# Optimization experiments

Measured on AMD Instinct MI355X. Metric: run time of the kernel, lower is better.

Reference implementation:

```python
import jax, jax.numpy as jnp
import numpy as np

EMB_DIM = 768
HEAD = 12
HEAD_DIM = EMB_DIM // HEAD


def setup_inputs() -> dict:
    key = jax.random.key(0)
    ks = jax.random.split(key, 6)
    B, N, D = 8, 1024, EMB_DIM
    s = 1.0 / np.sqrt(D)
    return {
        "z": jax.random.normal(ks[0], (B, N, D), dtype=jnp.float32),
        "w_q": jax.random.normal(ks[1], (D, D), dtype=jnp.float32) * s,
        "w_k": jax.random.normal(ks[2], (D, D), dtype=jnp.float32) * s,
        "w_v": jax.random.normal(ks[3], (D, D), dtype=jnp.float32) * s,
        "w_o": jax.random.normal(ks[4], (D, D), dtype=jnp.float32) * s,
        "b_o": jax.random.normal(ks[5], (D,), dtype=jnp.float32) * 0.01,
    }


def reference(z, w_q, w_k, w_v, w_o, b_o):
    B, N, D = z.shape
    sqrt_dh = jnp.asarray(HEAD_DIM, z.dtype) ** 0.5
    # project and split heads: [B, H, N, Dh]
    def heads(x, w):
        return (x @ w.T).reshape(B, N, HEAD, HEAD_DIM).transpose(0, 2, 1, 3)
    q = heads(z, w_q)
    k = heads(z, w_k)
    v = heads(z, w_v)
    dots = jnp.einsum("bhqd,bhkd->bhqk", q, k) / sqrt_dh
    attn = jax.nn.softmax(dots, axis=-1)  # dropout p=0 -> identity
    out = jnp.einsum("bhqk,bhkd->bhqd", attn, v)
    out = out.transpose(0, 2, 1, 3).reshape(B, N, D)
    return out @ w_o.T + b_o
```

## Files before the change

kernel.cpp:

```cpp
#include <hip/hip_runtime.h>
#include <hip/hip_bf16.h>
#include <stdint.h>

typedef unsigned short u16;
typedef __attribute__((ext_vector_type(8))) short bf16x8;
typedef __attribute__((ext_vector_type(4))) float f32x4;

__device__ __forceinline__ u16 f2bf(float f) {
    union { float f; unsigned int i; } c; c.f = f;
    unsigned int x = c.i;
    return (u16)((x + 0x7FFFu + ((x >> 16) & 1u)) >> 16);
}
__device__ __forceinline__ u16 f2bf_fast(float f) {
    union { float f; unsigned int i; } c; c.f = f;
    return (u16)((c.i + 0x8000u) >> 16);
}

__device__ __forceinline__ void glds16(const u16* g, u16* l) {
    __builtin_amdgcn_global_load_lds(
        (const __attribute__((address_space(1))) void*)g,
        (__attribute__((address_space(3))) void*)l, 16, 0, 0);
}

__device__ __forceinline__ void bar() { asm volatile("s_barrier" ::: "memory"); }
template <int N> __device__ __forceinline__ void waitv() {
    if constexpr (N == 0)      asm volatile("s_waitcnt vmcnt(0)" ::: "memory");
    else if constexpr (N == 2) asm volatile("s_waitcnt vmcnt(2)" ::: "memory");
    else if constexpr (N == 3) asm volatile("s_waitcnt vmcnt(3)" ::: "memory");
    else if constexpr (N == 4) asm volatile("s_waitcnt vmcnt(4)" ::: "memory");
    else if constexpr (N == 8) asm volatile("s_waitcnt vmcnt(8)" ::: "memory");
}

__global__ __launch_bounds__(256) void convert_all(
    const float* __restrict__ z, const float* __restrict__ wq,
    const float* __restrict__ wk, const float* __restrict__ wv,
    const float* __restrict__ wo,
    u16* __restrict__ zb, u16* __restrict__ wqb, u16* __restrict__ wkb,
    u16* __restrict__ wvb, u16* __restrict__ wob)
{
    int g = blockIdx.x * 256 + threadIdx.x;
    const float* s; u16* d;
    if (g < 786432)       { s = z;  d = zb;  }
    else if (g < 860160)  { s = wq; d = wqb; g -= 786432; }
    else if (g < 933888)  { s = wk; d = wkb; g -= 860160; }
    else if (g < 1007616) { s = wv; d = wvb; g -= 933888; }
    else                  { s = wo; d = wob; g -= 1007616; }
    float4 a = *(const float4*)(s + (size_t)g * 8);
    float4 b = *(const float4*)(s + (size_t)g * 8 + 4);
    u16 t[8] = {f2bf(a.x), f2bf(a.y), f2bf(a.z), f2bf(a.w),
                f2bf(b.x), f2bf(b.y), f2bf(b.z), f2bf(b.w)};
    *(uint4*)(d + (size_t)g * 8) = *(const uint4*)t;
}

template <int MI>
__device__ __forceinline__ void gemm_mainloop(
    const u16* __restrict__ A, const u16* __restrict__ B,
    u16* As, u16* Bs, f32x4 (&acc)[MI][4], int m0, int lda, int ldb, int K)
{
    const int t = threadIdx.x;
    const int w = t >> 6, lane = t & 63, quad = lane >> 4, lc = lane & 15;
    const int wm = w >> 1, wn = w & 1;
    const int swz = (lc >> 1) & 3;
    constexpr int NA = MI / 2;
    constexpr int ASZ = 1024 * MI;

    const u16* pa[NA]; int la[NA];
    #pragma unroll
    for (int j = 0; j < NA; j++) {
        const int c = j * 256 + t;
        const int row = c >> 2;
        const int kq = (c & 3) ^ ((row >> 1) & 3);
        pa[j] = &A[(size_t)(m0 + row) * lda + kq * 8];
        la[j] = (j * 256 + w * 64) * 8;
    }
    const u16* pb[2]; int lb[2];
    #pragma unroll
    for (int j = 0; j < 2; j++) {
        const int c = j * 256 + t;
        const int row = c >> 2;
        const int kq = (c & 3) ^ ((row >> 1) & 3);
        pb[j] = &B[(size_t)row * ldb + kq * 8];
        lb[j] = (j * 256 + w * 64) * 8;
    }

    #pragma unroll
    for (int j = 0; j < NA; j++) glds16(pa[j], As + la[j]);
    #pragma unroll
    for (int j = 0; j < 2; j++) glds16(pb[j], Bs + lb[j]);
    __syncthreads();

    int buf = 0;
    for (int k0 = 0; k0 < K; k0 += 32) {
        if (k0 + 32 < K) {
            const int na = (buf ^ 1) * ASZ, nbb = (buf ^ 1) * 4096;
            #pragma unroll
            for (int j = 0; j < NA; j++) glds16(pa[j] + k0 + 32, As + na + la[j]);
            #pragma unroll
            for (int j = 0; j < 2; j++)  glds16(pb[j] + k0 + 32, Bs + nbb + lb[j]);
        }
        bf16x8 af[MI], bfr[4];
        #pragma unroll
        for (int i = 0; i < MI; i++) {
            const int row = 32 * NA * wm + 16 * i + lc;
            af[i] = *(const bf16x8*)&As[buf * ASZ + (row * 4 + (quad ^ swz)) * 8];
        }
        #pragma unroll
        for (int j = 0; j < 4; j++) {
            const int row = 64 * wn + 16 * j + lc;
            bfr[j] = *(const bf16x8*)&Bs[buf * 4096 + (row * 4 + (quad ^ swz)) * 8];
        }
        #pragma unroll
        for (int i = 0; i < MI; i++)
            #pragma unroll
            for (int j = 0; j < 4; j++)
                acc[i][j] = __builtin_amdgcn_mfma_f32_16x16x32_bf16(af[i], bfr[j], acc[i][j], 0, 0, 0);
        __syncthreads();
        buf ^= 1;
    }
}

__global__ __launch_bounds__(256) void qkv_gemm(
    const u16* __restrict__ zb, const u16* __restrict__ wqb,
    const u16* __restrict__ wkb, const u16* __restrict__ wvb,
    u16* __restrict__ qkb, u16* __restrict__ vt)
{
    __shared__ __align__(16) u16 As[8192], Bs[8192];
    const int d = blockIdx.x;
    const int n0 = (d >> 6) * 128, m0 = (d & 63) * 128;
    const u16* Bp;
    if (n0 < 768)       Bp = wqb + (size_t)n0 * 768;
    else if (n0 < 1536) Bp = wkb + (size_t)(n0 - 768) * 768;
    else                Bp = wvb + (size_t)(n0 - 1536) * 768;

    const int t = threadIdx.x;
    const int w = t >> 6, lane = t & 63, quad = lane >> 4, lc = lane & 15;
    const int wm = w >> 1, wn = w & 1;
    const int swz = (lc >> 1) & 3;

    const u16* pa[2]; const u16* pb[2]; int la[2], lb[2];
    #pragma unroll
    for (int j = 0; j < 2; j++) {
        const int c = j * 256 + t;
        const int row = c >> 2;
        const int kq = (c & 3) ^ ((row >> 1) & 3);
        pa[j] = &zb[(size_t)(m0 + row) * 768 + kq * 8];
        pb[j] = &Bp[(size_t)row * 768 + kq * 8];
        la[j] = lb[j] = (j * 256 + w * 64) * 8;
    }

    glds16(pa[0], As + la[0]);  glds16(pa[1], As + la[1]);
    glds16(pb[0], Bs + lb[0]);  glds16(pb[1], Bs + lb[1]);
    glds16(pa[0] + 32, As + 4096 + la[0]);  glds16(pa[1] + 32, As + 4096 + la[1]);
    glds16(pb[0] + 32, Bs + 4096 + lb[0]);  glds16(pb[1] + 32, Bs + 4096 + lb[1]);

    f32x4 acc[4][4] = {};
    int buf = 0;
    for (int bk = 0; bk < 24; bk++) {
        if (bk + 1 < 24) waitv<4>(); else waitv<0>();
        bar();
        bf16x8 af[4], bfr[4];
        #pragma unroll
        for (int i = 0; i < 4; i++) {
            const int row = 64 * wm + 16 * i + lc;
            af[i] = *(const bf16x8*)&As[buf * 4096 + (row * 4 + (quad ^ swz)) * 8];
        }
        #pragma unroll
        for (int j = 0; j < 4; j++) {
            const int row = 64 * wn + 16 * j + lc;
            bfr[j] = *(const bf16x8*)&Bs[buf * 4096 + (row * 4 + (quad ^ swz)) * 8];
        }
        #pragma unroll
        for (int i = 0; i < 4; i++)
            #pragma unroll
            for (int j = 0; j < 4; j++)
                acc[i][j] = __builtin_amdgcn_mfma_f32_16x16x32_bf16(af[i], bfr[j], acc[i][j], 0, 0, 0);
        bar();
        if (bk + 2 < 24) {
            const int k2 = (bk + 2) * 32;
            glds16(pa[0] + k2, As + buf * 4096 + la[0]);
            glds16(pa[1] + k2, As + buf * 4096 + la[1]);
            glds16(pb[0] + k2, Bs + buf * 4096 + lb[0]);
            glds16(pb[1] + k2, Bs + buf * 4096 + lb[1]);
        }
        buf ^= 1;
    }

    if (n0 < 1536) {
        #pragma unroll
        for (int i = 0; i < 4; i++)
            #pragma unroll
            for (int j = 0; j < 4; j++) {
                const int col = n0 + 64 * wn + 16 * j + lc;
                #pragma unroll
                for (int r = 0; r < 4; r++) {
                    const int row = m0 + 64 * wm + 16 * i + quad * 4 + r;
                    qkb[(size_t)row * 1536 + col] = f2bf_fast(acc[i][j][r]);
                }
            }
    } else {
        #pragma unroll
        for (int i = 0; i < 4; i++)
            #pragma unroll
            for (int j = 0; j < 4; j++) {
                const int c = (n0 - 1536) + 64 * wn + 16 * j + lc;
                const int h = c >> 6, dd = c & 63;
                const int tok0 = m0 + 64 * wm + 16 * i + quad * 4;
                const int b = tok0 >> 10, n = tok0 & 1023;
                ushort4 pk = { f2bf_fast(acc[i][j][0]), f2bf_fast(acc[i][j][1]),
                               f2bf_fast(acc[i][j][2]), f2bf_fast(acc[i][j][3]) };
                *(ushort4*)&vt[(((size_t)(b * 12 + h)) * 64 + dd) * 1024 + n] = pk;
            }
    }
}

__global__ __launch_bounds__(256) void oproj_gemm(
    const u16* __restrict__ ob, const u16* __restrict__ wob,
    const float* __restrict__ bo, float* __restrict__ out)
{
    __shared__ __align__(16) u16 As[4096], Bs[8192];
    const int d = blockIdx.x;
    const int n0 = (d >> 7) * 128, m0 = (d & 127) * 64;
    f32x4 acc[2][4] = {};
    gemm_mainloop<2>(ob, wob + (size_t)n0 * 768, As, Bs, acc, m0, 768, 768, 768);

    const int t = threadIdx.x;
    const int w = t >> 6, lane = t & 63, quad = lane >> 4, lc = lane & 15;
    const int wm = w >> 1, wn = w & 1;
    #pragma unroll
    for (int i = 0; i < 2; i++)
        #pragma unroll
        for (int j = 0; j < 4; j++) {
            const int col = n0 + 64 * wn + 16 * j + lc;
            const float bv = bo[col];
            #pragma unroll
            for (int r = 0; r < 4; r++) {
                const int row = m0 + 32 * wm + 16 * i + quad * 4 + r;
                out[(size_t)row * 768 + col] = acc[i][j][r] + bv;
            }
        }
}

__global__ __launch_bounds__(256, 3) void attn_kernel(
    const u16* __restrict__ qkb, const u16* __restrict__ vt,
    u16* __restrict__ obuf)
{
    const int b = blockIdx.x / 12, h = blockIdx.x % 12;
    const int q0 = blockIdx.y * 128;
    const int t = threadIdx.x;
    const int w = t >> 6, lane = t & 63, quad = lane >> 4, lc = lane & 15;

    const u16* Qp  = qkb + (size_t)b * 1024 * 1536 + h * 64;
    const u16* Kp  = Qp + 768;
    const u16* Vtp = vt + ((size_t)(b * 12 + h)) * 64 * 1024;

    __shared__ __align__(16) u16 U[128 * 136];
    __shared__ __align__(16) u16 Vts[64 * 128];

    const u16* kp[4]; u16* kl[4];
    #pragma unroll
    for (int j = 0; j < 4; j++) {
        const int c = j * 256 + t;
        const int row = c >> 3;
        const int kq = (c & 7) ^ ((row >> 1) & 7);
        kp[j] = Kp + (size_t)row * 1536 + kq * 8;
        kl[j] = &U[(j * 256 + w * 64) * 8];
    }
    const u16* vp[4]; u16* vl[4];
    #pragma unroll
    for (int s2 = 0; s2 < 4; s2++) {
        const int s = 4 * w + s2;
        const int c = s * 64 + lane;
        const int dd = c >> 4, kq = (c & 15) ^ (dd & 15);
        vp[s2] = Vtp + (size_t)dd * 1024 + kq * 8;
        vl[s2] = &Vts[s * 512];
    }

    bf16x8 qf[2][2];
    #pragma unroll
    for (int rg = 0; rg < 2; rg++)
        #pragma unroll
        for (int kk = 0; kk < 2; kk++)
            qf[rg][kk] = *(const bf16x8*)&Qp[(size_t)(q0 + 32 * w + 16 * rg + lc) * 1536
                                             + kk * 32 + quad * 8];

    f32x4 oacc[2][4] = {};
    float lsum[2][4] = {};

    const float cs = 0.18033688011112042f;
    const int swk = (lc >> 1) & 7;

    waitv<0>();
    for (int kt = 0; kt < 8; kt++) {
        const int kb = kt * 128;
        bar();
        #pragma unroll
        for (int j = 0; j < 4; j++)
            glds16(kp[j] + (size_t)kb * 1536, kl[j]);
        #pragma unroll
        for (int s2 = 0; s2 < 4; s2++)
            glds16(vp[s2] + kb, vl[s2]);
        waitv<4>();
        bar();

        f32x4 sacc[2][8] = {};
        #pragma unroll
        for (int j = 0; j < 8; j++) {
            const int nrow = 16 * j + lc;
            bf16x8 kf0 = *(const bf16x8*)&U[(nrow * 8 + (quad ^ swk)) * 8];
            bf16x8 kf1 = *(const bf16x8*)&U[(nrow * 8 + ((4 + quad) ^ swk)) * 8];
            #pragma unroll
            for (int rg = 0; rg < 2; rg++) {
                sacc[rg][j] = __builtin_amdgcn_mfma_f32_16x16x32_bf16(qf[rg][0], kf0, sacc[rg][j], 0, 0, 0);
                sacc[rg][j] = __builtin_amdgcn_mfma_f32_16x16x32_bf16(qf[rg][1], kf1, sacc[rg][j], 0, 0, 0);
            }
        }
        waitv<0>();
        bar();

        #pragma unroll
        for (int rg = 0; rg < 2; rg++)
            #pragma unroll
            for (int j = 0; j < 8; j++)
                #pragma unroll
                for (int r = 0; r < 4; r++) {
                    float p = __builtin_amdgcn_exp2f(sacc[rg][j][r] * cs);
                    lsum[rg][r] += p;
                    U[(32 * w + 16 * rg + quad * 4 + r) * 136 + 16 * j + lc] = f2bf_fast(p);
                }

        #pragma unroll
        for (int ks = 0; ks < 4; ks++) {
            bf16x8 pa[2];
            #pragma unroll
            for (int rg = 0; rg < 2; rg++)
                pa[rg] = *(const bf16x8*)&U[(32 * w + 16 * rg + lc) * 136 + ks * 32 + quad * 8];
            #pragma unroll
            for (int jd = 0; jd < 4; jd++) {
                bf16x8 vb = *(const bf16x8*)&Vts[(((16 * jd + lc) << 4) + ((ks * 4 + quad) ^ lc)) * 8];
                #pragma unroll
                for (int rg = 0; rg < 2; rg++)
                    oacc[rg][jd] = __builtin_amdgcn_mfma_f32_16x16x32_bf16(pa[rg], vb, oacc[rg][jd], 0, 0, 0);
            }
        }
    }

    #pragma unroll
    for (int off = 1; off < 16; off <<= 1)
        #pragma unroll
        for (int rg = 0; rg < 2; rg++)
            #pragma unroll
            for (int r = 0; r < 4; r++)
                lsum[rg][r] += __shfl_xor(lsum[rg][r], off, 64);

    float invl[2][4];
    #pragma unroll
    for (int rg = 0; rg < 2; rg++)
        #pragma unroll
        for (int r = 0; r < 4; r++) invl[rg][r] = __builtin_amdgcn_rcpf(lsum[rg][r]);
    #pragma unroll
    for (int rg = 0; rg < 2; rg++)
        #pragma unroll
        for (int jd = 0; jd < 4; jd++)
            #pragma unroll
            for (int r = 0; r < 4; r++) {
                const int row = q0 + 32 * w + 16 * rg + quad * 4 + r;
                const int col = h * 64 + 16 * jd + lc;
                obuf[((size_t)b * 1024 + row) * 768 + col] = f2bf_fast(oacc[rg][jd][r] * invl[rg][r]);
            }
}

extern "C" void kernel_launch(void* const* d_in, const int* in_sizes, int n_in,
                              void* d_out, int out_size, void* d_ws, size_t ws_size,
                              hipStream_t stream) {
    const float* z  = (const float*)d_in[0];
    const float* wq = (const float*)d_in[1];
    const float* wk = (const float*)d_in[2];
    const float* wv = (const float*)d_in[3];
    const float* wo = (const float*)d_in[4];
    const float* bo = (const float*)d_in[5];

    u16* ws16 = (u16*)d_ws;
    u16* zb   = ws16;
    u16* wqb  = zb  + 6291456;
    u16* wkb  = wqb + 589824;
    u16* wvb  = wkb + 589824;
    u16* wob  = wvb + 589824;
    u16* vt   = wob + 589824;
    u16* qkb  = (u16*)d_out;
    u16* obuf = zb;
    float* out = (float*)d_out;

    convert_all<<<4224, 256, 0, stream>>>(z, wq, wk, wv, wo, zb, wqb, wkb, wvb, wob);
    qkv_gemm<<<1152, 256, 0, stream>>>(zb, wqb, wkb, wvb, qkb, vt);
    attn_kernel<<<dim3(96, 8), 256, 0, stream>>>(qkb, vt, obuf);
    oproj_gemm<<<768, 256, 0, stream>>>(obuf, wob, bo, out);
}
```

Before: 193.4 us.

## Shrink attention key tile to 64, double-buffer K, separate P buffer

The attention loop now processes 64-key tiles instead of 128 and double-buffers K in shared memory, prefetching the next K tile while the current one is used. P gets its own XOR-swizzled buffer instead of aliasing the K staging area, and the V tile layout is adjusted to match the smaller tile. Shared memory per block drops, and launch bounds are raised to 4 blocks per CU for more occupancy. This adds twice as many loop iterations and barriers and tighter register pressure.

```diff
diff --git a/kernel.cpp b/kernel.cpp
--- a/kernel.cpp
+++ b/kernel.cpp
@@ -240,7 +240,7 @@
         }
 }
 
-__global__ __launch_bounds__(256, 3) void attn_kernel(
+__global__ __launch_bounds__(256, 4) void attn_kernel(
     const u16* __restrict__ qkb, const u16* __restrict__ vt,
     u16* __restrict__ obuf)
 {
@@ -253,24 +253,25 @@
     const u16* Kp  = Qp + 768;
     const u16* Vtp = vt + ((size_t)(b * 12 + h)) * 64 * 1024;
 
-    __shared__ __align__(16) u16 U[128 * 136];
-    __shared__ __align__(16) u16 Vts[64 * 128];
-
-    const u16* kp[4]; u16* kl[4];
-    #pragma unroll
-    for (int j = 0; j < 4; j++) {
+    __shared__ __align__(16) u16 Ks[2][4096];
+    __shared__ __align__(16) u16 Vts[4096];
+    __shared__ __align__(16) u16 Ps[8192];
+
+    const u16* kp[2]; int kl[2];
+    #pragma unroll
+    for (int j = 0; j < 2; j++) {
         const int c = j * 256 + t;
         const int row = c >> 3;
         const int kq = (c & 7) ^ ((row >> 1) & 7);
         kp[j] = Kp + (size_t)row * 1536 + kq * 8;
-        kl[j] = &U[(j * 256 + w * 64) * 8];
-    }
-    const u16* vp[4]; u16* vl[4];
-    #pragma unroll
-    for (int s2 = 0; s2 < 4; s2++) {
-        const int s = 4 * w + s2;
+        kl[j] = (j * 256 + w * 64) * 8;
+    }
+    const u16* vp[2]; u16* vl[2];
+    #pragma unroll
+    for (int s2 = 0; s2 < 2; s2++) {
+        const int s = 2 * w + s2;
         const int c = s * 64 + lane;
-        const int dd = c >> 4, kq = (c & 15) ^ (dd & 15);
+        const int dd = c >> 3, kq = (c & 7) ^ (dd & 7);
         vp[s2] = Vtp + (size_t)dd * 1024 + kq * 8;
         vl[s2] = &Vts[s * 512];
     }
@@ -288,55 +289,72 @@
 
     const float cs = 0.18033688011112042f;
     const int swk = (lc >> 1) & 7;
+    const int pR0 = 32 * w;
 
     waitv<0>();
-    for (int kt = 0; kt < 8; kt++) {
-        const int kb = kt * 128;
+    glds16(kp[0], &Ks[0][0] + kl[0]);
+    glds16(kp[1], &Ks[0][0] + kl[1]);
+
+    for (int kt = 0; kt < 16; kt++) {
+        const int kb = kt * 64;
         bar();
-        #pragma unroll
-        for (int j = 0; j < 4; j++)
-            glds16(kp[j] + (size_t)kb * 1536, kl[j]);
-        #pragma unroll
-        for (int s2 = 0; s2 < 4; s2++)
-            glds16(vp[s2] + kb, vl[s2]);
-        waitv<4>();
+        glds16(vp[0] + kb, vl[0]);
+        glds16(vp[1] + kb, vl[1]);
+        if (kt + 1 < 16) {
+            const size_t kb1 = (size_t)(kt + 1) * 64 * 1536;
+            u16* kd = &Ks[(kt + 1) & 1][0];
+            glds16(kp[0] + kb1, kd + kl[0]);
+            glds16(kp[1] + kb1, kd + kl[1]);
+            waitv<4>();
+        } else {
+            waitv<2>();
+        }
         bar();
 
-        f32x4 sacc[2][8] = {};
-        #pragma unroll
-        for (int j = 0; j < 8; j++) {
+        const u16* Kc = &Ks[kt & 1][0];
+        f32x4 sacc[2][4] = {};
+        #pragma unroll
+        for (int j = 0; j < 4; j++) {
             const int nrow = 16 * j + lc;
-            bf16x8 kf0 = *(const bf16x8*)&U[(nrow * 8 + (quad ^ swk)) * 8];
-            bf16x8 kf1 = *(const bf16x8*)&U[(nrow * 8 + ((4 + quad) ^ swk)) * 8];
+            bf16x8 kf0 = *(const bf16x8*)&Kc[(nrow * 8 + (quad ^ swk)) * 8];
+            bf16x8 kf1 = *(const bf16x8*)&Kc[(nrow * 8 + ((4 + quad) ^ swk)) * 8];
             #pragma unroll
             for (int rg = 0; rg < 2; rg++) {
                 sacc[rg][j] = __builtin_amdgcn_mfma_f32_16x16x32_bf16(qf[rg][0], kf0, sacc[rg][j], 0, 0, 0);
                 sacc[rg][j] = __builtin_amdgcn_mfma_f32_16x16x32_bf16(qf[rg][1], kf1, sacc[rg][j], 0, 0, 0);
             }
         }
-        waitv<0>();
+        if (kt + 1 < 16) waitv<2>();
+        else             waitv<0>();
         bar();
 
         #pragma unroll
-        for (int rg = 0; rg < 2; rg++)
-            #pragma unroll
-            for (int j = 0; j < 8; j++)
+        for (int rg = 0; rg < 2; rg++) {
+            const int Rb = pR0 + 16 * rg + quad * 4;
+            #pragma unroll
+            for (int j = 0; j < 4; j++)
                 #pragma unroll
                 for (int r = 0; r < 4; r++) {
                     float p = __builtin_amdgcn_exp2f(sacc[rg][j][r] * cs);
                     lsum[rg][r] += p;
-                    U[(32 * w + 16 * rg + quad * 4 + r) * 136 + 16 * j + lc] = f2bf_fast(p);
+                    const int R = Rb + r;
+                    const int slot = (2 * j + (lc >> 3)) ^ ((R >> 1) & 7);
+                    Ps[R * 64 + slot * 8 + (lc & 7)] = f2bf_fast(p);
                 }
-
-        #pragma unroll
-        for (int ks = 0; ks < 4; ks++) {
+        }
+
+        #pragma unroll
+        for (int ks = 0; ks < 2; ks++) {
             bf16x8 pa[2];
             #pragma unroll
-            for (int rg = 0; rg < 2; rg++)
-                pa[rg] = *(const bf16x8*)&U[(32 * w + 16 * rg + lc) * 136 + ks * 32 + quad * 8];
+            for (int rg = 0; rg < 2; rg++) {
+                const int Rp = pR0 + 16 * rg + lc;
+                pa[rg] = *(const bf16x8*)&Ps[Rp * 64 + (((ks * 4 + quad) ^ ((Rp >> 1) & 7)) << 3)];
+            }
             #pragma unroll
             for (int jd = 0; jd < 4; jd++) {
-                bf16x8 vb = *(const bf16x8*)&Vts[(((16 * jd + lc) << 4) + ((ks * 4 + quad) ^ lc)) * 8];
+                const int dd = 16 * jd + lc;
+                bf16x8 vb = *(const bf16x8*)&Vts[(dd * 8 + ((ks * 4 + quad) ^ (dd & 7))) * 8];
                 #pragma unroll
                 for (int rg = 0; rg < 2; rg++)
                     oacc[rg][jd] = __builtin_amdgcn_mfma_f32_16x16x32_bf16(pa[rg], vb, oacc[rg][jd], 0, 0, 0);
```

Result: no change. 197.0 us (+1.9%).
